# Optimization experiments

Hardware: AMD Instinct MI355X
Metric: run time of the kernel (lower is better)

Reference implementation:

```python
import jax, jax.numpy as jnp
import numpy as np

B, S, IN_DIM, HID, K, NUM_STEPS = 8, 4096, 64, 512, 3, 12


def setup_inputs() -> dict:
    key = jax.random.key(0)
    ks = jax.random.split(key, 7)
    scale_in = 1.0 / np.sqrt(IN_DIM)
    scale_conv = 1.0 / np.sqrt(HID * K)
    scale_out = 1.0 / np.sqrt(HID)
    return {
        "x": jax.random.normal(ks[0], (B, S, IN_DIM), dtype=jnp.float32),
        "W_in": jax.random.normal(ks[1], (IN_DIM, HID), dtype=jnp.float32) * scale_in,
        "b_in": jnp.zeros((HID,), dtype=jnp.float32),
        "W_conv": jax.random.normal(ks[2], (HID, HID, K), dtype=jnp.float32) * scale_conv,
        "b_conv": jnp.zeros((HID,), dtype=jnp.float32),
        "W_out": jax.random.normal(ks[3], (HID, IN_DIM), dtype=jnp.float32) * scale_out,
        "b_out": jnp.zeros((IN_DIM,), dtype=jnp.float32),
    }


def reference(x, W_in, b_in, W_conv, b_conv, W_out, b_out):
    # input projection: (B, S, IN) @ (IN, HID) -> (B, S, HID)
    h = x @ W_in + b_in
    # to channels-first: (B, HID, S)
    h = jnp.transpose(h, (0, 2, 1))
    dn = jax.lax.conv_dimension_numbers(h.shape, W_conv.shape, ("NCH", "OIH", "NCH"))
    pad = K // 2

    def step(h_state, _):
        c = jax.lax.conv_general_dilated(
            h_state, W_conv, window_strides=(1,), padding=[(pad, pad)],
            dimension_numbers=dn)
        c = c + b_conv[None, :, None]
        return jax.nn.relu(c), None

    h, _ = jax.lax.scan(step, h, None, length=NUM_STEPS)
    # back to (B, S, HID), then output projection
    h = jnp.transpose(h, (0, 2, 1))
    return h @ W_out + b_out
```

## Files before the change

### kernel.cpp

```cpp
#include <hip/hip_runtime.h>

#define B_ 8
#define S_ 4096
#define IN_ 64
#define HID_ 512
#define NSTEP 12
#define SP_ (S_ + 2)
#define NP_ (B_ * SP_)
#define NTOT (B_ * S_)

typedef unsigned short u16;
typedef __attribute__((ext_vector_type(8))) short bf16x8;
typedef __attribute__((ext_vector_type(4))) float f32x4;

__device__ __forceinline__ u16 f2bf(float f) {
  unsigned u = __float_as_uint(f);
  u += 0x7fffu + ((u >> 16) & 1u);
  return (u16)(u >> 16);
}

__device__ __forceinline__ void gload16(const void* g, void* l) {
  __builtin_amdgcn_global_load_lds((const __attribute__((address_space(1))) void*)g,
                                   (__attribute__((address_space(3))) void*)l, 16, 0, 0);
}

__global__ void setup_kernel(const float* __restrict__ x, const float* __restrict__ Wc,
                             const float* __restrict__ Wi, const float* __restrict__ Wo,
                             u16* __restrict__ wcb, u16* __restrict__ wib,
                             u16* __restrict__ wob, u16* __restrict__ xbf,
                             u16* __restrict__ h0, u16* __restrict__ h1) {
  const int n_wc = 3 * HID_ * HID_;
  const int n_wio = IN_ * HID_;
  const int n_xb = NTOT * IN_;
  const int n_pad = 2 * B_ * 2 * HID_;
  const long total = (long)n_wc + 2 * n_wio + n_xb + n_pad;
  for (long u = (long)blockIdx.x * blockDim.x + threadIdx.x; u < total;
       u += (long)gridDim.x * blockDim.x) {
    long v = u;
    if (v < n_wc) {
      int k = (int)(v / (HID_ * HID_));
      int rem = (int)(v % (HID_ * HID_));
      int o = rem / HID_, i = rem % HID_;
      wcb[v] = f2bf(Wc[((long)o * HID_ + i) * 3 + k]);
    } else if ((v -= n_wc) < n_wio) {
      int i = (int)(v / IN_), j = (int)(v % IN_);
      wib[v] = f2bf(Wi[j * HID_ + i]);
    } else if ((v -= n_wio) < n_wio) {
      int j = (int)(v / HID_), i = (int)(v % HID_);
      wob[v] = f2bf(Wo[i * IN_ + j]);
    } else if ((v -= n_wio) < n_xb) {
      xbf[v] = f2bf(x[v]);
    } else {
      v -= n_xb;
      int buf = (int)(v / (B_ * 2 * HID_));
      int r = (int)(v % (B_ * 2 * HID_));
      int b = r / (2 * HID_);
      int q = r % (2 * HID_);
      int side = q / HID_, i = q % HID_;
      long p = (long)b * SP_ + (side ? (S_ + 1) : 0);
      (buf ? h1 : h0)[p * HID_ + i] = 0;
    }
  }
}

__global__ __launch_bounds__(256, 2) void proj_in_gemm(const u16* __restrict__ xb,
                                                       const u16* __restrict__ wib,
                                                       const float* __restrict__ bin,
                                                       u16* __restrict__ hout) {
  __shared__ __align__(16) u16 Ab[128 * 64];
  __shared__ __align__(16) u16 Bb[128 * 64];
  const int tid = threadIdx.x, wid = tid >> 6, lane = tid & 63;
  const int nt = blockIdx.x, mt = blockIdx.y;
  const int wr = wid >> 1, wcn = wid & 1, fr = lane & 15, fq = lane >> 4;
#pragma unroll
  for (int c = 0; c < 4; ++c) {
    const int ch = wid * 4 + c;
    const int row = ch * 8 + (lane >> 3), cb = (lane & 7) * 8;
    gload16(wib + (mt * 128 + row) * 64 + cb, &Ab[ch * 512]);
    gload16(xb + ((long)nt * 128 + row) * 64 + cb, &Bb[ch * 512]);
  }
  f32x4 acc[4][4];
#pragma unroll
  for (int m = 0; m < 4; ++m)
#pragma unroll
    for (int n = 0; n < 4; ++n) acc[m][n] = {0.f, 0.f, 0.f, 0.f};
  __syncthreads();
#pragma unroll
  for (int t = 0; t < 2; ++t) {
    const int j0 = t * 32;
    bf16x8 af[4], bfv[4];
#pragma unroll
    for (int m = 0; m < 4; ++m)
      af[m] = *(const bf16x8*)&Ab[(wr * 64 + m * 16 + fr) * 64 + j0 + fq * 8];
#pragma unroll
    for (int n = 0; n < 4; ++n)
      bfv[n] = *(const bf16x8*)&Bb[(wcn * 64 + n * 16 + fr) * 64 + j0 + fq * 8];
#pragma unroll
    for (int m = 0; m < 4; ++m)
#pragma unroll
      for (int n = 0; n < 4; ++n)
        acc[m][n] = __builtin_amdgcn_mfma_f32_16x16x32_bf16(af[m], bfv[n], acc[m][n], 0, 0, 0);
  }
  const int n0 = nt * 128;
  const int bb = n0 / S_, s0v = n0 % S_;
  const int prow = bb * SP_ + s0v + 1;
#pragma unroll
  for (int m = 0; m < 4; ++m) {
    const int i = mt * 128 + wr * 64 + m * 16 + fq * 4;
    const float4 bias = *(const float4*)&bin[i];
#pragma unroll
    for (int n = 0; n < 4; ++n) {
      const int nl = wcn * 64 + n * 16 + fr;
      const long p = prow + nl;
      union { u16 q[4]; uint2 v; } u;
      u.q[0] = f2bf(acc[m][n][0] + bias.x);
      u.q[1] = f2bf(acc[m][n][1] + bias.y);
      u.q[2] = f2bf(acc[m][n][2] + bias.z);
      u.q[3] = f2bf(acc[m][n][3] + bias.w);
      *(uint2*)&hout[p * HID_ + i] = u.v;
    }
  }
}

__global__ __launch_bounds__(512, 2) void conv_gemm3(const u16* __restrict__ hin,
                                                     u16* __restrict__ hout,
                                                     const u16* __restrict__ wcb,
                                                     const float* __restrict__ bconv) {
  extern __shared__ __align__(16) u16 smem[];
  const int tid = threadIdx.x;
  const int w = tid >> 6, lane = tid & 63;
  const int wm = w >> 2, wn = w & 3;
  const int fr = lane & 15, fq = lane >> 4;
  const int mbase = blockIdx.y * 256;
  const int n0 = blockIdx.x * 256;
  const int bb = n0 / S_, s0 = n0 % S_;
  const int prow0 = bb * SP_ + s0;

  const int tl = (tid * 16) ^ (((tid >> 3) & 3) << 4);
  const int srow = tl >> 6;
  const int scol = (tl & 63) >> 1;
  const int wdst = w * 1024;

  auto stage = [&](int dbuf, int u) {
    const int kk = u % 3;
    const int i0 = (u / 3) * 32;
    char* base = (char*)smem + (size_t)dbuf * 32768;
    const u16* ga = wcb + (size_t)kk * (HID_ * HID_) + (size_t)(mbase + srow) * HID_ + i0 + scol;
    const u16* gb = hin + (size_t)(prow0 + kk + srow) * HID_ + i0 + scol;
    gload16(ga, base + wdst);
    gload16(ga + 128 * HID_, base + 8192 + wdst);
    gload16(gb, base + 16384 + wdst);
    gload16(gb + 128 * HID_, base + 24576 + wdst);
  };

  f32x4 acc[8][4];
#pragma unroll
  for (int m = 0; m < 8; ++m)
#pragma unroll
    for (int n = 0; n < 4; ++n) acc[m][n] = {0.f, 0.f, 0.f, 0.f};

  stage(0, 0);
  stage(1, 1);
  stage(2, 2);

  const int swzb = ((fr >> 1) & 3) << 4;
  const int aoffs = (((wm * 128 + fr) * 64 + fq * 16)) ^ swzb;
  const int boffs = (((wn * 64 + fr) * 64 + fq * 16)) ^ swzb;

#pragma unroll 12
  for (int t = 0; t < 48; ++t) {
    const int buf = t & 3;
    const char* A = (const char*)smem + (size_t)buf * 32768;
    const char* Bv = A + 16384;

    asm volatile("s_waitcnt vmcnt(8)" ::: "memory");
    __builtin_amdgcn_sched_barrier(0);
    __builtin_amdgcn_s_barrier();
    __builtin_amdgcn_sched_barrier(0);

    bf16x8 af[8], bfv[4];
#pragma unroll
    for (int m = 0; m < 4; ++m)
      af[m] = *(const bf16x8*)(A + aoffs + m * 1024);
#pragma unroll
    for (int n = 0; n < 4; ++n)
      bfv[n] = *(const bf16x8*)(Bv + boffs + n * 1024);
    __builtin_amdgcn_sched_barrier(0);
    {
      int u = t + 3;
      if (u > 47) u = 47;
      stage((t + 3) & 3, u);
    }
    __builtin_amdgcn_sched_barrier(0);
#pragma unroll
    for (int m = 4; m < 8; ++m)
      af[m] = *(const bf16x8*)(A + aoffs + m * 1024);
    __builtin_amdgcn_sched_barrier(0);

    asm volatile("s_waitcnt lgkmcnt(4)" ::: "memory");
    __builtin_amdgcn_sched_barrier(0);
    __builtin_amdgcn_s_setprio(1);
#pragma unroll
    for (int m = 0; m < 4; ++m)
#pragma unroll
      for (int n = 0; n < 4; ++n)
        acc[m][n] = __builtin_amdgcn_mfma_f32_16x16x32_bf16(af[m], bfv[n], acc[m][n], 0, 0, 0);
    __builtin_amdgcn_s_setprio(0);
    __builtin_amdgcn_sched_barrier(0);

    asm volatile("s_waitcnt lgkmcnt(0)" ::: "memory");
    __builtin_amdgcn_sched_barrier(0);
    __builtin_amdgcn_s_setprio(1);
#pragma unroll
    for (int m = 4; m < 8; ++m)
#pragma unroll
      for (int n = 0; n < 4; ++n)
        acc[m][n] = __builtin_amdgcn_mfma_f32_16x16x32_bf16(af[m], bfv[n], acc[m][n], 0, 0, 0);
    __builtin_amdgcn_s_setprio(0);
    __builtin_amdgcn_sched_barrier(0);
  }

#pragma unroll
  for (int m = 0; m < 8; ++m) {
    const int o = mbase + wm * 128 + m * 16 + fq * 4;
    const float4 bias = *(const float4*)&bconv[o];
#pragma unroll
    for (int n = 0; n < 4; ++n) {
      const int nl = wn * 64 + n * 16 + fr;
      const long p = (long)prow0 + 1 + nl;
      union { u16 q[4]; uint2 v; } u;
      u.q[0] = f2bf(fmaxf(acc[m][n][0] + bias.x, 0.f));
      u.q[1] = f2bf(fmaxf(acc[m][n][1] + bias.y, 0.f));
      u.q[2] = f2bf(fmaxf(acc[m][n][2] + bias.z, 0.f));
      u.q[3] = f2bf(fmaxf(acc[m][n][3] + bias.w, 0.f));
      *(uint2*)&hout[p * HID_ + o] = u.v;
    }
  }
}

__global__ __launch_bounds__(256, 2) void proj_out_gemm(const u16* __restrict__ hin,
                                                        const u16* __restrict__ wob,
                                                        const float* __restrict__ bout,
                                                        float* __restrict__ out) {
  __shared__ __align__(16) u16 Ab[2][128 * 32];
  __shared__ __align__(16) u16 Bb[2][64 * 32];
  const int tid = threadIdx.x, wid = tid >> 6, lane = tid & 63;
  const int nt = blockIdx.x;
  const int bb = (nt * 128) / S_, s0v = (nt * 128) % S_;
  const int prow0 = bb * SP_ + s0v + 1;
  const int l4 = lane >> 2, lb = (lane & 3) * 8;
  const int fr = lane & 15, fq = lane >> 4;

  f32x4 acc[2][4];
#pragma unroll
  for (int m = 0; m < 2; ++m)
#pragma unroll
    for (int n = 0; n < 4; ++n) acc[m][n] = {0.f, 0.f, 0.f, 0.f};

  auto stage = [&](int buf, int t) {
    const int i0 = t * 32;
#pragma unroll
    for (int c = 0; c < 2; ++c) {
      const int ch = wid * 2 + c;
      gload16(hin + (long)(prow0 + ch * 16 + l4) * HID_ + i0 + lb, &Ab[buf][ch * 512]);
    }
    gload16(wob + (wid * 16 + l4) * HID_ + i0 + lb, &Bb[buf][wid * 512]);
  };

  stage(0, 0);
  __syncthreads();
  for (int t = 0; t < 16; ++t) {
    const int cur = t & 1;
    if (t < 15) stage(cur ^ 1, t + 1);
    bf16x8 af[2], bfv[4];
#pragma unroll
    for (int m = 0; m < 2; ++m)
      af[m] = *(const bf16x8*)&Ab[cur][(wid * 32 + m * 16 + fr) * 32 + fq * 8];
#pragma unroll
    for (int j = 0; j < 4; ++j)
      bfv[j] = *(const bf16x8*)&Bb[cur][(j * 16 + fr) * 32 + fq * 8];
#pragma unroll
    for (int m = 0; m < 2; ++m)
#pragma unroll
      for (int j = 0; j < 4; ++j)
        acc[m][j] = __builtin_amdgcn_mfma_f32_16x16x32_bf16(af[m], bfv[j], acc[m][j], 0, 0, 0);
    __syncthreads();
  }
  const int n0 = nt * 128;
#pragma unroll
  for (int m = 0; m < 2; ++m) {
    const int nbase = n0 + wid * 32 + m * 16 + fq * 4;
#pragma unroll
    for (int jf = 0; jf < 4; ++jf) {
      const int j = jf * 16 + fr;
      const float bj = bout[j];
#pragma unroll
      for (int r = 0; r < 4; ++r)
        out[(long)(nbase + r) * IN_ + j] = acc[m][jf][r] + bj;
    }
  }
}

extern "C" void kernel_launch(void* const* d_in, const int* in_sizes, int n_in,
                              void* d_out, int out_size, void* d_ws, size_t ws_size,
                              hipStream_t stream) {
  (void)in_sizes; (void)n_in; (void)out_size; (void)ws_size;
  const float* x = (const float*)d_in[0];
  const float* W_in = (const float*)d_in[1];
  const float* b_in = (const float*)d_in[2];
  const float* W_conv = (const float*)d_in[3];
  const float* b_conv = (const float*)d_in[4];
  const float* W_out = (const float*)d_in[5];
  const float* b_out = (const float*)d_in[6];
  float* out = (float*)d_out;
  char* ws = (char*)d_ws;

  const size_t hbytes = (size_t)NP_ * HID_ * sizeof(u16);
  u16* h0 = (u16*)ws;
  u16* h1 = (u16*)(ws + hbytes);
  u16* wcb = (u16*)(ws + 2 * hbytes);
  u16* wib = (u16*)(ws + 2 * hbytes + (size_t)3 * HID_ * HID_ * 2);
  u16* wob = (u16*)(ws + 2 * hbytes + ((size_t)3 * HID_ * HID_ + IN_ * HID_) * 2);
  u16* xbf = (u16*)(ws + 2 * hbytes + ((size_t)3 * HID_ * HID_ + 2 * IN_ * HID_) * 2);

  static int lds_attr_set = 0;
  if (!lds_attr_set) {
    (void)hipFuncSetAttribute((const void*)conv_gemm3,
                              hipFuncAttributeMaxDynamicSharedMemorySize, 131072);
    lds_attr_set = 1;
  }

  setup_kernel<<<2048, 256, 0, stream>>>(x, W_conv, W_in, W_out, wcb, wib, wob, xbf, h0, h1);
  proj_in_gemm<<<dim3(NTOT / 128, HID_ / 128), 256, 0, stream>>>(xbf, wib, b_in, h0);
  const u16* cin = h0;
  u16* cout = h1;
  for (int s = 0; s < NSTEP; ++s) {
    conv_gemm3<<<dim3(NTOT / 256, 2), 512, 131072, stream>>>(cin, cout, wcb, b_conv);
    u16* t = (u16*)cin; cin = cout; cout = t;
  }
  proj_out_gemm<<<NTOT / 128, 256, 0, stream>>>(cin, wob, b_out, out);
}
```

Baseline: 590.0 us.

## Switch conv GEMM to 32x32x16 MFMA with fragment-ordered LDS staging

Replaces the 16x16x32 bf16 MFMA tiles in the conv kernel with 32x32x16 MFMA, so each wave issues fewer, larger matrix instructions per k-step. The global-to-LDS staging is reorganized so each 1 KB LDS chunk holds one 32-row fragment already laid out in lane order, removing the XOR swizzle and letting each lane read its operand at a fixed lane*16 offset. The epilogue is rewritten for the 32x32 accumulator layout. The aim is higher MFMA throughput and fewer LDS reads per FLOP, at the risk of LDS bank conflicts or worse latency hiding with the new layout and wait counts.

```diff
diff --git a/kernel.cpp b/kernel.cpp
--- a/kernel.cpp
+++ b/kernel.cpp
@@ -12,6 +12,7 @@
 typedef unsigned short u16;
 typedef __attribute__((ext_vector_type(8))) short bf16x8;
 typedef __attribute__((ext_vector_type(4))) float f32x4;
+typedef __attribute__((ext_vector_type(16))) float f32x16;
 
 __device__ __forceinline__ u16 f2bf(float f) {
   unsigned u = __float_as_uint(f);
@@ -122,7 +123,7 @@
   }
 }
 
-__global__ __launch_bounds__(512, 2) void conv_gemm3(const u16* __restrict__ hin,
+__global__ __launch_bounds__(512, 2) void conv_gemm6(const u16* __restrict__ hin,
                                                      u16* __restrict__ hout,
                                                      const u16* __restrict__ wcb,
                                                      const float* __restrict__ bconv) {
@@ -130,81 +131,82 @@
   const int tid = threadIdx.x;
   const int w = tid >> 6, lane = tid & 63;
   const int wm = w >> 2, wn = w & 3;
-  const int fr = lane & 15, fq = lane >> 4;
+  const int r32 = lane & 31, khi = lane >> 5;
   const int mbase = blockIdx.y * 256;
   const int n0 = blockIdx.x * 256;
   const int bb = n0 / S_, s0 = n0 % S_;
   const int prow0 = bb * SP_ + s0;
 
-  const int tl = (tid * 16) ^ (((tid >> 3) & 3) << 4);
-  const int srow = tl >> 6;
-  const int scol = (tl & 63) >> 1;
-  const int wdst = w * 1024;
-
-  auto stage = [&](int dbuf, int u) {
+  const int voff = r32 * HID_ + khi * 8;
+
+  auto stage = [&](int u) {
+    if (u > 47) u = 47;
     const int kk = u % 3;
     const int i0 = (u / 3) * 32;
-    char* base = (char*)smem + (size_t)dbuf * 32768;
-    const u16* ga = wcb + (size_t)kk * (HID_ * HID_) + (size_t)(mbase + srow) * HID_ + i0 + scol;
-    const u16* gb = hin + (size_t)(prow0 + kk + srow) * HID_ + i0 + scol;
-    gload16(ga, base + wdst);
-    gload16(ga + 128 * HID_, base + 8192 + wdst);
-    gload16(gb, base + 16384 + wdst);
-    gload16(gb + 128 * HID_, base + 24576 + wdst);
+    char* base = (char*)smem + (u & 3) * 32768;
+#pragma unroll
+    for (int c = 0; c < 4; ++c) {
+      const int fid = w * 4 + c;
+      const u16* g;
+      if (fid < 16) {
+        const int mfb = fid >> 1, kh = fid & 1;
+        g = wcb + (size_t)kk * (HID_ * HID_) + (size_t)(mbase + mfb * 32) * HID_ + i0 + kh * 16 + voff;
+      } else {
+        const int fb = fid - 16, nfb = fb >> 1, kh = fb & 1;
+        g = hin + (size_t)(prow0 + kk + nfb * 32) * HID_ + i0 + kh * 16 + voff;
+      }
+      gload16(g, base + fid * 1024);
+    }
   };
 
-  f32x4 acc[8][4];
-#pragma unroll
-  for (int m = 0; m < 8; ++m)
-#pragma unroll
-    for (int n = 0; n < 4; ++n) acc[m][n] = {0.f, 0.f, 0.f, 0.f};
-
-  stage(0, 0);
-  stage(1, 1);
-  stage(2, 2);
-
-  const int swzb = ((fr >> 1) & 3) << 4;
-  const int aoffs = (((wm * 128 + fr) * 64 + fq * 16)) ^ swzb;
-  const int boffs = (((wn * 64 + fr) * 64 + fq * 16)) ^ swzb;
+  f32x16 acc[4][2];
+#pragma unroll
+  for (int mf = 0; mf < 4; ++mf)
+#pragma unroll
+    for (int nf = 0; nf < 2; ++nf)
+#pragma unroll
+      for (int e = 0; e < 16; ++e) acc[mf][nf][e] = 0.f;
+
+  const int abase = wm * 8192 + lane * 16;
+  const int bbase = 16384 + wn * 4096 + lane * 16;
+
+  stage(0); stage(1); stage(2);
 
 #pragma unroll 12
   for (int t = 0; t < 48; ++t) {
-    const int buf = t & 3;
-    const char* A = (const char*)smem + (size_t)buf * 32768;
-    const char* Bv = A + 16384;
+    const char* bufp = (const char*)smem + (t & 3) * 32768;
 
     asm volatile("s_waitcnt vmcnt(8)" ::: "memory");
     __builtin_amdgcn_sched_barrier(0);
     __builtin_amdgcn_s_barrier();
     __builtin_amdgcn_sched_barrier(0);
 
-    bf16x8 af[8], bfv[4];
-#pragma unroll
-    for (int m = 0; m < 4; ++m)
-      af[m] = *(const bf16x8*)(A + aoffs + m * 1024);
-#pragma unroll
-    for (int n = 0; n < 4; ++n)
-      bfv[n] = *(const bf16x8*)(Bv + boffs + n * 1024);
-    __builtin_amdgcn_sched_barrier(0);
-    {
-      int u = t + 3;
-      if (u > 47) u = 47;
-      stage((t + 3) & 3, u);
-    }
-    __builtin_amdgcn_sched_barrier(0);
-#pragma unroll
-    for (int m = 4; m < 8; ++m)
-      af[m] = *(const bf16x8*)(A + aoffs + m * 1024);
-    __builtin_amdgcn_sched_barrier(0);
-
-    asm volatile("s_waitcnt lgkmcnt(4)" ::: "memory");
+    bf16x8 af0[4], bf0[2], af1[4], bf1[2];
+#pragma unroll
+    for (int mf = 0; mf < 4; ++mf)
+      af0[mf] = *(const bf16x8*)(bufp + abase + (mf * 2 + 0) * 1024);
+#pragma unroll
+    for (int nf = 0; nf < 2; ++nf)
+      bf0[nf] = *(const bf16x8*)(bufp + bbase + (nf * 2 + 0) * 1024);
+    __builtin_amdgcn_sched_barrier(0);
+    stage(t + 3);
+    __builtin_amdgcn_sched_barrier(0);
+#pragma unroll
+    for (int mf = 0; mf < 4; ++mf)
+      af1[mf] = *(const bf16x8*)(bufp + abase + (mf * 2 + 1) * 1024);
+#pragma unroll
+    for (int nf = 0; nf < 2; ++nf)
+      bf1[nf] = *(const bf16x8*)(bufp + bbase + (nf * 2 + 1) * 1024);
+    __builtin_amdgcn_sched_barrier(0);
+
+    asm volatile("s_waitcnt lgkmcnt(6)" ::: "memory");
     __builtin_amdgcn_sched_barrier(0);
     __builtin_amdgcn_s_setprio(1);
 #pragma unroll
-    for (int m = 0; m < 4; ++m)
-#pragma unroll
-      for (int n = 0; n < 4; ++n)
-        acc[m][n] = __builtin_amdgcn_mfma_f32_16x16x32_bf16(af[m], bfv[n], acc[m][n], 0, 0, 0);
+    for (int mf = 0; mf < 4; ++mf)
+#pragma unroll
+      for (int nf = 0; nf < 2; ++nf)
+        acc[mf][nf] = __builtin_amdgcn_mfma_f32_32x32x16_bf16(af0[mf], bf0[nf], acc[mf][nf], 0, 0, 0);
     __builtin_amdgcn_s_setprio(0);
     __builtin_amdgcn_sched_barrier(0);
 
@@ -212,30 +214,32 @@
     __builtin_amdgcn_sched_barrier(0);
     __builtin_amdgcn_s_setprio(1);
 #pragma unroll
-    for (int m = 4; m < 8; ++m)
-#pragma unroll
-      for (int n = 0; n < 4; ++n)
-        acc[m][n] = __builtin_amdgcn_mfma_f32_16x16x32_bf16(af[m], bfv[n], acc[m][n], 0, 0, 0);
+    for (int mf = 0; mf < 4; ++mf)
+#pragma unroll
+      for (int nf = 0; nf < 2; ++nf)
+        acc[mf][nf] = __builtin_amdgcn_mfma_f32_32x32x16_bf16(af1[mf], bf1[nf], acc[mf][nf], 0, 0, 0);
     __builtin_amdgcn_s_setprio(0);
     __builtin_amdgcn_sched_barrier(0);
   }
 
 #pragma unroll
-  for (int m = 0; m < 8; ++m) {
-    const int o = mbase + wm * 128 + m * 16 + fq * 4;
-    const float4 bias = *(const float4*)&bconv[o];
-#pragma unroll
-    for (int n = 0; n < 4; ++n) {
-      const int nl = wn * 64 + n * 16 + fr;
-      const long p = (long)prow0 + 1 + nl;
-      union { u16 q[4]; uint2 v; } u;
-      u.q[0] = f2bf(fmaxf(acc[m][n][0] + bias.x, 0.f));
-      u.q[1] = f2bf(fmaxf(acc[m][n][1] + bias.y, 0.f));
-      u.q[2] = f2bf(fmaxf(acc[m][n][2] + bias.z, 0.f));
-      u.q[3] = f2bf(fmaxf(acc[m][n][3] + bias.w, 0.f));
-      *(uint2*)&hout[p * HID_ + o] = u.v;
-    }
-  }
+  for (int mf = 0; mf < 4; ++mf)
+#pragma unroll
+    for (int g = 0; g < 4; ++g) {
+      const int o = mbase + wm * 128 + mf * 32 + g * 8 + khi * 4;
+      const float4 bias = *(const float4*)&bconv[o];
+#pragma unroll
+      for (int nf = 0; nf < 2; ++nf) {
+        const int n = wn * 64 + nf * 32 + r32;
+        const long p = (long)prow0 + 1 + n;
+        union { u16 q[4]; uint2 v; } uo;
+        uo.q[0] = f2bf(fmaxf(acc[mf][nf][g * 4 + 0] + bias.x, 0.f));
+        uo.q[1] = f2bf(fmaxf(acc[mf][nf][g * 4 + 1] + bias.y, 0.f));
+        uo.q[2] = f2bf(fmaxf(acc[mf][nf][g * 4 + 2] + bias.z, 0.f));
+        uo.q[3] = f2bf(fmaxf(acc[mf][nf][g * 4 + 3] + bias.w, 0.f));
+        *(uint2*)&hout[p * HID_ + o] = uo.v;
+      }
+    }
 }
 
 __global__ __launch_bounds__(256, 2) void proj_out_gemm(const u16* __restrict__ hin,
@@ -325,7 +329,7 @@
 
   static int lds_attr_set = 0;
   if (!lds_attr_set) {
-    (void)hipFuncSetAttribute((const void*)conv_gemm3,
+    (void)hipFuncSetAttribute((const void*)conv_gemm6,
                               hipFuncAttributeMaxDynamicSharedMemorySize, 131072);
     lds_attr_set = 1;
   }
@@ -335,7 +339,7 @@
   const u16* cin = h0;
   u16* cout = h1;
   for (int s = 0; s < NSTEP; ++s) {
-    conv_gemm3<<<dim3(NTOT / 256, 2), 512, 131072, stream>>>(cin, cout, wcb, b_conv);
+    conv_gemm6<<<dim3(NTOT / 256, 2), 512, 131072, stream>>>(cin, cout, wcb, b_conv);
     u16* t = (u16*)cin; cin = cout; cout = t;
   }
   proj_out_gemm<<<NTOT / 128, 256, 0, stream>>>(cin, wob, b_out, out);
```

Result: slower. 759.6 us (+28.8%).
